# Kernel optimization log

Hardware: AMD Instinct MI355X
Metric: run time of the kernel (lower is better)

The kernel has to match this reference:

```python
import jax, jax.numpy as jnp
import numpy as np

L, H, P_LOC = 32768, 512, 256  # seq len, in/out dim, local state dim (conj_sym: P//2)
DT_MIN, DT_MAX = 1e-3, 1e-1
STEP_RESCALE = 1.0


def setup_inputs() -> dict:
    key = jax.random.key(0)
    ks = jax.random.split(key, 10)
    # stable eigenvalues: negative real part (mimics HiPPO init real part -1/2)
    Lambda_re = -0.1 - jax.random.uniform(ks[0], (P_LOC,), dtype=jnp.float32)
    Lambda_im = jax.random.normal(ks[1], (P_LOC,), dtype=jnp.float32) * jnp.pi
    B_re = jax.random.normal(ks[2], (P_LOC, H), dtype=jnp.float32) / jnp.sqrt(2.0 * H)
    B_im = jax.random.normal(ks[3], (P_LOC, H), dtype=jnp.float32) / jnp.sqrt(2.0 * H)
    C_re = jax.random.normal(ks[4], (H, P_LOC), dtype=jnp.float32) / jnp.sqrt(2.0 * P_LOC)
    C_im = jax.random.normal(ks[5], (H, P_LOC), dtype=jnp.float32) / jnp.sqrt(2.0 * P_LOC)
    D = jax.random.normal(ks[6], (H,), dtype=jnp.float32)
    u01 = jax.random.uniform(ks[7], (P_LOC,), dtype=jnp.float32)
    log_step = u01 * (jnp.log(DT_MAX) - jnp.log(DT_MIN)) + jnp.log(DT_MIN)
    input_sequence = jax.random.normal(ks[8], (L, H), dtype=jnp.float32)
    integration_timesteps = jax.random.uniform(ks[9], (L,), dtype=jnp.float32)
    return {
        "input_sequence": input_sequence,
        "integration_timesteps": integration_timesteps,
        "Lambda_re": Lambda_re, "Lambda_im": Lambda_im,
        "B_re": B_re, "B_im": B_im,
        "C_re": C_re, "C_im": C_im,
        "D": D, "log_step": log_step,
    }


def _binop(q_i, q_j):
    A_i, b_i = q_i
    A_j, b_j = q_j
    return (A_j * A_i, A_j * b_i + b_j)


def reference(input_sequence, integration_timesteps, Lambda_re, Lambda_im,
              B_re, B_im, C_re, C_im, D, log_step):
    Lambda = Lambda_re + 1j * Lambda_im          # (P,)
    B = B_re + 1j * B_im                         # (P, H)
    C_tilde = C_re + 1j * C_im                   # (H, P)
    step = STEP_RESCALE * jnp.exp(log_step)      # (P,)
    # ZOH discretization per timestep: Delta[l,p] = step[p] * dt[l]
    Delta = integration_timesteps[:, None] * step[None, :]          # (L, P)
    Lambda_bar = jnp.exp(Lambda[None, :] * Delta)                   # (L, P) complex
    gamma_bar = (Lambda_bar - 1.0) / Lambda[None, :]                # (L, P) complex
    Bu = gamma_bar * jnp.einsum("lh,ph->lp", input_sequence.astype(B.dtype), B)
    _, xs = jax.lax.associative_scan(_binop, (Lambda_bar, Bu))      # (L, P)
    # conj_sym=True -> output is 2 * Re(C x)
    ys = 2.0 * jnp.einsum("lp,hp->lh", xs, C_tilde).real            # (L, H)
    return ys + D[None, :] * input_sequence
```

## Files before the change

kernel.cpp:

```cpp
#include <hip/hip_runtime.h>
#include <math.h>

#define L_SEQ 32768
#define H_DIM 512
#define P_DIM 256
#define K_DIM 512
#define CHUNK 32
#define NCHUNK (L_SEQ / CHUNK)

typedef __bf16 bf16x8 __attribute__((ext_vector_type(8)));
typedef float floatx4 __attribute__((ext_vector_type(4)));

__device__ __forceinline__ void gll16(const void* g, void* l) {
    __builtin_amdgcn_global_load_lds(
        (__attribute__((address_space(1))) void*)(g),
        (__attribute__((address_space(3))) void*)(l), 16, 0, 0);
}

__global__ __launch_bounds__(512) void build_b2_kernel(
    const float* __restrict__ Bre, const float* __restrict__ Bim,
    __bf16* __restrict__ B2)
{
    const int p = blockIdx.x;
    const int h = threadIdx.x;
    B2[(2 * p) * 512 + h]     = (__bf16)Bre[p * H_DIM + h];
    B2[(2 * p + 1) * 512 + h] = (__bf16)Bim[p * H_DIM + h];
}

__global__ __launch_bounds__(256) void build_c2_kernel(
    const float* __restrict__ Cre, const float* __restrict__ Cim,
    __bf16* __restrict__ C2)
{
    const int h = blockIdx.x;
    const int p = threadIdx.x;
    C2[h * 512 + 2 * p]     = (__bf16)Cre[h * P_DIM + p];
    C2[h * 512 + 2 * p + 1] = (__bf16)(-Cim[h * P_DIM + p]);
}

__global__ __launch_bounds__(256) void gemm1_kernel(
    const float* __restrict__ A,
    const __bf16* __restrict__ Bm,
    __bf16* __restrict__ Out)
{
    __shared__ float  Asf[128 * 32];
    __shared__ __bf16 Bs [128 * 32];

    const int tid = threadIdx.x;
    const int w  = tid >> 6;
    const int ln = tid & 63;
    const int bm = blockIdx.x;
    const int bn = blockIdx.y;

    floatx4 acc[4][4];
    #pragma unroll
    for (int i = 0; i < 4; ++i)
        #pragma unroll
        for (int j = 0; j < 4; ++j)
            acc[i][j] = (floatx4){0.f, 0.f, 0.f, 0.f};

    const int a_r = ln >> 3;
    const int a_c = (ln & 7) << 2;
    const int b_r = ln >> 2;
    const int b_c = (ln & 3) << 3;
    const size_t brow = (size_t)(bn * 128 + w * 16 + b_r) * K_DIM;

    float*  lA[4];
    size_t  gAr[4];
    #pragma unroll
    for (int q = 0; q < 4; ++q) {
        lA[q] = Asf + (q * 32 + w * 8) * 32;
        gAr[q] = (size_t)(bm * 128 + q * 32 + w * 8 + a_r) * K_DIM;
    }
    __bf16* lB0 = Bs + w * 512;
    __bf16* lB1 = Bs + 2048 + w * 512;

    const int wm = (w >> 1) * 64;
    const int wn = (w & 1) * 64;
    const int fr = ln & 15;
    const int fq = (ln >> 4) * 8;

    for (int kt = 0; kt < K_DIM; kt += 32) {
        __syncthreads();
        #pragma unroll
        for (int q = 0; q < 4; ++q)
            gll16(A + gAr[q] + kt + a_c, lA[q]);
        gll16(Bm + brow + kt + b_c,                      lB0);
        gll16(Bm + brow + (size_t)64 * K_DIM + kt + b_c, lB1);
        __syncthreads();

        bf16x8 a[4], b[4];
        #pragma unroll
        for (int mt = 0; mt < 4; ++mt) {
            floatx4 a0 = *(floatx4*)&Asf[(wm + mt * 16 + fr) * 32 + fq];
            floatx4 a1 = *(floatx4*)&Asf[(wm + mt * 16 + fr) * 32 + fq + 4];
            #pragma unroll
            for (int r = 0; r < 4; ++r) {
                a[mt][r]     = (__bf16)a0[r];
                a[mt][4 + r] = (__bf16)a1[r];
            }
        }
        #pragma unroll
        for (int nt = 0; nt < 4; ++nt)
            b[nt] = *(bf16x8*)&Bs[(wn + nt * 16 + fr) * 32 + fq];

        #pragma unroll
        for (int mt = 0; mt < 4; ++mt)
            #pragma unroll
            for (int nt = 0; nt < 4; ++nt)
                acc[mt][nt] = __builtin_amdgcn_mfma_f32_16x16x32_bf16(
                    a[mt], b[nt], acc[mt][nt], 0, 0, 0);
    }

    const int rq = (ln >> 4) * 4;
    #pragma unroll
    for (int mt = 0; mt < 4; ++mt) {
        const int gro = bm * 128 + wm + mt * 16 + rq;
        #pragma unroll
        for (int nt = 0; nt < 4; ++nt) {
            const int gco = bn * 128 + wn + nt * 16 + (ln & 15);
            #pragma unroll
            for (int r = 0; r < 4; ++r)
                Out[(size_t)(gro + r) * 512 + gco] = (__bf16)acc[mt][nt][r];
        }
    }
}

__global__ __launch_bounds__(256) void gemm2_kernel(
    const __bf16* __restrict__ A,
    const __bf16* __restrict__ Bm,
    float* __restrict__ Out,
    const float* __restrict__ U,
    const float* __restrict__ Dv)
{
    __shared__ __bf16 As[128 * 32];
    __shared__ __bf16 Bs[128 * 32];

    const int tid = threadIdx.x;
    const int w  = tid >> 6;
    const int ln = tid & 63;
    const int bm = blockIdx.x;
    const int bn = blockIdx.y;

    floatx4 acc[4][4];
    #pragma unroll
    for (int i = 0; i < 4; ++i)
        #pragma unroll
        for (int j = 0; j < 4; ++j)
            acc[i][j] = (floatx4){0.f, 0.f, 0.f, 0.f};

    const int lr = ln >> 2;
    const int lce = (ln & 3) << 3;
    const size_t arow = (size_t)(bm * 128 + w * 16 + lr) * K_DIM;
    const size_t brow = (size_t)(bn * 128 + w * 16 + lr) * K_DIM;

    __bf16* lA0 = As + w * 512;
    __bf16* lA1 = As + 2048 + w * 512;
    __bf16* lB0 = Bs + w * 512;
    __bf16* lB1 = Bs + 2048 + w * 512;

    const int wm = (w >> 1) * 64;
    const int wn = (w & 1) * 64;
    const int fr = ln & 15;
    const int fq = (ln >> 4) * 8;

    for (int kt = 0; kt < K_DIM; kt += 32) {
        __syncthreads();
        gll16(A  + arow + kt + lce,                      lA0);
        gll16(A  + arow + (size_t)64 * K_DIM + kt + lce, lA1);
        gll16(Bm + brow + kt + lce,                      lB0);
        gll16(Bm + brow + (size_t)64 * K_DIM + kt + lce, lB1);
        __syncthreads();

        bf16x8 a[4], b[4];
        #pragma unroll
        for (int mt = 0; mt < 4; ++mt)
            a[mt] = *(bf16x8*)&As[(wm + mt * 16 + fr) * 32 + fq];
        #pragma unroll
        for (int nt = 0; nt < 4; ++nt)
            b[nt] = *(bf16x8*)&Bs[(wn + nt * 16 + fr) * 32 + fq];

        #pragma unroll
        for (int mt = 0; mt < 4; ++mt)
            #pragma unroll
            for (int nt = 0; nt < 4; ++nt)
                acc[mt][nt] = __builtin_amdgcn_mfma_f32_16x16x32_bf16(
                    a[mt], b[nt], acc[mt][nt], 0, 0, 0);
    }

    const int rq = (ln >> 4) * 4;
    #pragma unroll
    for (int mt = 0; mt < 4; ++mt) {
        const int gro = bm * 128 + wm + mt * 16 + rq;
        #pragma unroll
        for (int nt = 0; nt < 4; ++nt) {
            const int gco = bn * 128 + wn + nt * 16 + (ln & 15);
            const float dh = Dv[gco];
            #pragma unroll
            for (int r = 0; r < 4; ++r) {
                const size_t o = (size_t)(gro + r) * 512 + gco;
                Out[o] = 2.0f * acc[mt][nt][r] + dh * U[o];
            }
        }
    }
}

template <int WRITE_X>
__global__ __launch_bounds__(256) void scan_chunk_kernel(
    const float* __restrict__ dts,
    const float* __restrict__ Lre_g, const float* __restrict__ Lim_g,
    const float* __restrict__ logstep,
    unsigned int* __restrict__ G2u,
    float4* __restrict__ Agg,
    const float2* __restrict__ Carry)
{
    const int p = threadIdx.x;
    const int c = blockIdx.x;
    const int base = c * CHUNK;

    unsigned int g[CHUNK];
    float dt[CHUNK];
    #pragma unroll
    for (int i = 0; i < CHUNK; ++i)
        g[i] = G2u[(size_t)(base + i) * 256 + p];
    #pragma unroll
    for (int i = 0; i < CHUNK; ++i)
        dt[i] = dts[base + i];

    const float lre = Lre_g[p];
    const float lim = Lim_g[p];
    const float stp = __expf(logstep[p]);
    const float inv_den = 1.0f / (lre * lre + lim * lim);

    float Are = 1.0f, Aim = 0.0f;
    float xre, xim;
    if (WRITE_X) {
        float2 cc = Carry[c * P_DIM + p];
        xre = cc.x; xim = cc.y;
    } else {
        xre = 0.0f; xim = 0.0f;
    }

    #pragma unroll
    for (int i = 0; i < CHUNK; ++i) {
        const float d = stp * dt[i];
        const float er = __expf(lre * d);
        float sn, cs;
        __sincosf(lim * d, &sn, &cs);
        const float are = er * cs;
        const float aim = er * sn;
        const float am1 = are - 1.0f;
        const float gr = (am1 * lre + aim * lim) * inv_den;
        const float gi = (aim * lre - am1 * lim) * inv_den;

        const float ure = __uint_as_float(g[i] << 16);
        const float uim = __uint_as_float(g[i] & 0xffff0000u);
        const float bre = gr * ure - gi * uim;
        const float bim = gr * uim + gi * ure;

        const float nxre = are * xre - aim * xim + bre;
        const float nxim = are * xim + aim * xre + bim;
        xre = nxre; xim = nxim;

        if (WRITE_X) {
            __bf16 xr = (__bf16)xre;
            __bf16 xi = (__bf16)xim;
            unsigned int o = (unsigned int)*(unsigned short*)&xr |
                             ((unsigned int)*(unsigned short*)&xi << 16);
            G2u[(size_t)(base + i) * 256 + p] = o;
        } else {
            const float nAre = are * Are - aim * Aim;
            const float nAim = are * Aim + aim * Are;
            Are = nAre; Aim = nAim;
        }
    }

    if (!WRITE_X)
        Agg[p * NCHUNK + c] = make_float4(Are, Aim, xre, xim);
}

__global__ __launch_bounds__(1024) void carry_kernel(
    const float4* __restrict__ Agg,
    float2* __restrict__ Carry)
{
    const int p = blockIdx.x;
    const int c = threadIdx.x;

    __shared__ float sAr[NCHUNK], sAi[NCHUNK], sBr[NCHUNK], sBi[NCHUNK];

    float4 v = Agg[p * NCHUNK + c];
    float ar = v.x, ai = v.y, br = v.z, bi = v.w;
    sAr[c] = ar; sAi[c] = ai; sBr[c] = br; sBi[c] = bi;
    __syncthreads();

    #pragma unroll
    for (int off = 1; off < NCHUNK; off <<= 1) {
        float par, pai, pbr, pbi;
        const bool act = (c >= off);
        if (act) {
            par = sAr[c - off]; pai = sAi[c - off];
            pbr = sBr[c - off]; pbi = sBi[c - off];
        }
        __syncthreads();
        if (act) {
            const float nbr = ar * pbr - ai * pbi + br;
            const float nbi = ar * pbi + ai * pbr + bi;
            const float nar = ar * par - ai * pai;
            const float nai = ar * pai + ai * par;
            ar = nar; ai = nai; br = nbr; bi = nbi;
            sAr[c] = ar; sAi[c] = ai; sBr[c] = br; sBi[c] = bi;
        }
        __syncthreads();
    }

    float cr = 0.0f, ci = 0.0f;
    if (c > 0) { cr = sBr[c - 1]; ci = sBi[c - 1]; }
    Carry[c * P_DIM + p] = make_float2(cr, ci);
}

extern "C" void kernel_launch(void* const* d_in, const int* in_sizes, int n_in,
                              void* d_out, int out_size, void* d_ws, size_t ws_size,
                              hipStream_t stream) {
    const float* U       = (const float*)d_in[0];
    const float* dts     = (const float*)d_in[1];
    const float* Lre     = (const float*)d_in[2];
    const float* Lim     = (const float*)d_in[3];
    const float* Bre     = (const float*)d_in[4];
    const float* Bim     = (const float*)d_in[5];
    const float* Cre     = (const float*)d_in[6];
    const float* Cim     = (const float*)d_in[7];
    const float* Dv      = (const float*)d_in[8];
    const float* logstep = (const float*)d_in[9];
    float* out = (float*)d_out;

    char* ws = (char*)d_ws;
    __bf16* G2 = (__bf16*)ws;
    __bf16* B2 = (__bf16*)(ws + (size_t)L_SEQ * 512 * 2);
    __bf16* C2 = B2 + 512 * 512;
    float4* Agg = (float4*)(C2 + 512 * 512);
    float2* Carry = (float2*)(Agg + (size_t)P_DIM * NCHUNK);

    build_b2_kernel<<<P_DIM, 512, 0, stream>>>(Bre, Bim, B2);
    build_c2_kernel<<<H_DIM, 256, 0, stream>>>(Cre, Cim, C2);

    dim3 g1(L_SEQ / 128, 4);
    gemm1_kernel<<<g1, 256, 0, stream>>>(U, B2, G2);

    unsigned int* G2u = (unsigned int*)G2;
    scan_chunk_kernel<0><<<NCHUNK, 256, 0, stream>>>(
        dts, Lre, Lim, logstep, G2u, Agg, nullptr);
    carry_kernel<<<P_DIM, NCHUNK, 0, stream>>>(Agg, Carry);
    scan_chunk_kernel<1><<<NCHUNK, 256, 0, stream>>>(
        dts, Lre, Lim, logstep, G2u, nullptr, Carry);

    dim3 g2(L_SEQ / 128, 4);
    gemm2_kernel<<<g2, 256, 0, stream>>>(G2, C2, out, U, Dv);
}
```

Measured before the change: 231.2 us.

## Replace LDS carry scan with wavefront shuffle scan and merge build kernels

```diff
diff --git a/kernel.cpp b/kernel.cpp
--- a/kernel.cpp
+++ b/kernel.cpp
@@ -17,24 +17,24 @@
         (__attribute__((address_space(3))) void*)(l), 16, 0, 0);
 }
 
-__global__ __launch_bounds__(512) void build_b2_kernel(
+__global__ __launch_bounds__(512) void build_kernel(
     const float* __restrict__ Bre, const float* __restrict__ Bim,
-    __bf16* __restrict__ B2)
-{
-    const int p = blockIdx.x;
-    const int h = threadIdx.x;
-    B2[(2 * p) * 512 + h]     = (__bf16)Bre[p * H_DIM + h];
-    B2[(2 * p + 1) * 512 + h] = (__bf16)Bim[p * H_DIM + h];
-}
-
-__global__ __launch_bounds__(256) void build_c2_kernel(
     const float* __restrict__ Cre, const float* __restrict__ Cim,
-    __bf16* __restrict__ C2)
-{
-    const int h = blockIdx.x;
-    const int p = threadIdx.x;
-    C2[h * 512 + 2 * p]     = (__bf16)Cre[h * P_DIM + p];
-    C2[h * 512 + 2 * p + 1] = (__bf16)(-Cim[h * P_DIM + p]);
+    __bf16* __restrict__ B2, __bf16* __restrict__ C2)
+{
+    const int b = blockIdx.x;
+    const int t = threadIdx.x;
+    if (b < 256) {
+        B2[(2 * b) * 512 + t]     = (__bf16)Bre[b * H_DIM + t];
+        B2[(2 * b + 1) * 512 + t] = (__bf16)Bim[b * H_DIM + t];
+    } else {
+        const int h = b - 256;
+        const int p = t & 255;
+        if (t < 256)
+            C2[h * 512 + 2 * p]     = (__bf16)Cre[h * P_DIM + p];
+        else
+            C2[h * 512 + 2 * p + 1] = (__bf16)(-Cim[h * P_DIM + p]);
+    }
 }
 
 __global__ __launch_bounds__(256) void gemm1_kernel(
@@ -278,43 +278,71 @@
         Agg[p * NCHUNK + c] = make_float4(Are, Aim, xre, xim);
 }
 
-__global__ __launch_bounds__(1024) void carry_kernel(
+struct CT { float Ar, Ai, br, bi; };
+
+__device__ __forceinline__ CT ct_compose(const CT& f, const CT& s) {
+    CT r;
+    r.Ar = s.Ar * f.Ar - s.Ai * f.Ai;
+    r.Ai = s.Ar * f.Ai + s.Ai * f.Ar;
+    r.br = s.Ar * f.br - s.Ai * f.bi + s.br;
+    r.bi = s.Ar * f.bi + s.Ai * f.br + s.bi;
+    return r;
+}
+
+__global__ __launch_bounds__(256) void carry_shfl_kernel(
     const float4* __restrict__ Agg,
     float2* __restrict__ Carry)
 {
-    const int p = blockIdx.x;
-    const int c = threadIdx.x;
-
-    __shared__ float sAr[NCHUNK], sAi[NCHUNK], sBr[NCHUNK], sBi[NCHUNK];
-
-    float4 v = Agg[p * NCHUNK + c];
-    float ar = v.x, ai = v.y, br = v.z, bi = v.w;
-    sAr[c] = ar; sAi[c] = ai; sBr[c] = br; sBi[c] = bi;
+    const int pch = blockIdx.x;
+    const int t  = threadIdx.x;
+    const int ln = t & 63;
+    const int wv = t >> 6;
+
+    __shared__ float4 wtot[4];
+
+    CT v[4];
+    #pragma unroll
+    for (int i = 0; i < 4; ++i) {
+        float4 f = Agg[(size_t)pch * NCHUNK + 4 * t + i];
+        v[i].Ar = f.x; v[i].Ai = f.y; v[i].br = f.z; v[i].bi = f.w;
+    }
+    CT val = v[0];
+    #pragma unroll
+    for (int i = 1; i < 4; ++i) val = ct_compose(val, v[i]);
+
+    #pragma unroll
+    for (int off = 1; off < 64; off <<= 1) {
+        CT o;
+        o.Ar = __shfl_up(val.Ar, off);
+        o.Ai = __shfl_up(val.Ai, off);
+        o.br = __shfl_up(val.br, off);
+        o.bi = __shfl_up(val.bi, off);
+        if (ln >= off) val = ct_compose(o, val);
+    }
+
+    CT lexcl;
+    lexcl.Ar = __shfl_up(val.Ar, 1);
+    lexcl.Ai = __shfl_up(val.Ai, 1);
+    lexcl.br = __shfl_up(val.br, 1);
+    lexcl.bi = __shfl_up(val.bi, 1);
+    if (ln == 0) { lexcl.Ar = 1.f; lexcl.Ai = 0.f; lexcl.br = 0.f; lexcl.bi = 0.f; }
+
+    if (ln == 63) wtot[wv] = make_float4(val.Ar, val.Ai, val.br, val.bi);
     __syncthreads();
 
-    #pragma unroll
-    for (int off = 1; off < NCHUNK; off <<= 1) {
-        float par, pai, pbr, pbi;
-        const bool act = (c >= off);
-        if (act) {
-            par = sAr[c - off]; pai = sAi[c - off];
-            pbr = sBr[c - off]; pbi = sBi[c - off];
-        }
-        __syncthreads();
-        if (act) {
-            const float nbr = ar * pbr - ai * pbi + br;
-            const float nbi = ar * pbi + ai * pbr + bi;
-            const float nar = ar * par - ai * pai;
-            const float nai = ar * pai + ai * par;
-            ar = nar; ai = nai; br = nbr; bi = nbi;
-            sAr[c] = ar; sAi[c] = ai; sBr[c] = br; sBi[c] = bi;
-        }
-        __syncthreads();
-    }
-
-    float cr = 0.0f, ci = 0.0f;
-    if (c > 0) { cr = sBr[c - 1]; ci = sBi[c - 1]; }
-    Carry[c * P_DIM + p] = make_float2(cr, ci);
+    CT wpre; wpre.Ar = 1.f; wpre.Ai = 0.f; wpre.br = 0.f; wpre.bi = 0.f;
+    for (int i = 0; i < wv; ++i) {
+        float4 f = wtot[i];
+        CT tt; tt.Ar = f.x; tt.Ai = f.y; tt.br = f.z; tt.bi = f.w;
+        wpre = ct_compose(wpre, tt);
+    }
+
+    CT E = ct_compose(wpre, lexcl);
+    #pragma unroll
+    for (int i = 0; i < 4; ++i) {
+        Carry[(size_t)(4 * t + i) * P_DIM + pch] = make_float2(E.br, E.bi);
+        E = ct_compose(E, v[i]);
+    }
 }
 
 extern "C" void kernel_launch(void* const* d_in, const int* in_sizes, int n_in,
@@ -339,8 +367,7 @@
     float4* Agg = (float4*)(C2 + 512 * 512);
     float2* Carry = (float2*)(Agg + (size_t)P_DIM * NCHUNK);
 
-    build_b2_kernel<<<P_DIM, 512, 0, stream>>>(Bre, Bim, B2);
-    build_c2_kernel<<<H_DIM, 256, 0, stream>>>(Cre, Cim, C2);
+    build_kernel<<<768, 512, 0, stream>>>(Bre, Bim, Cre, Cim, B2, C2);
 
     dim3 g1(L_SEQ / 128, 4);
     gemm1_kernel<<<g1, 256, 0, stream>>>(U, B2, G2);
@@ -348,7 +375,7 @@
     unsigned int* G2u = (unsigned int*)G2;
     scan_chunk_kernel<0><<<NCHUNK, 256, 0, stream>>>(
         dts, Lre, Lim, logstep, G2u, Agg, nullptr);
-    carry_kernel<<<P_DIM, NCHUNK, 0, stream>>>(Agg, Carry);
+    carry_shfl_kernel<<<P_DIM, 256, 0, stream>>>(Agg, Carry);
     scan_chunk_kernel<1><<<NCHUNK, 256, 0, stream>>>(
         dts, Lre, Lim, logstep, G2u, nullptr, Carry);
 
```

New measurement: 228.3 us. No clear change (-1.3%).
